# Kernel tuning notes

Hardware: AMD Instinct MI355X
Metric: run time of the kernel (lower is better)

Reference implementation:

```python
import jax, jax.numpy as jnp
import numpy as np
from jax import lax

B, T, H, E, V, ENC = 2048, 48, 512, 256, 128, 1024


def setup_inputs() -> dict:
    key = jax.random.key(0)
    ks = jax.random.split(key, 13)
    s = 0.05  # weight scale to keep activations sane
    return {
        "tgt_ids": jax.random.randint(ks[0], (B, T), 0, V),
        "enc_hid": jax.random.normal(ks[1], (B, ENC), jnp.float32),
        "W_init1": s * jax.random.normal(ks[2], (ENC, H), jnp.float32),
        "W_init2": s * jax.random.normal(ks[3], (ENC, H), jnp.float32),
        "embed_table": s * jax.random.normal(ks[4], (V, E), jnp.float32),
        "k1": s * jax.random.normal(ks[5], (E, 3 * H), jnp.float32),
        "rk1": s * jax.random.normal(ks[6], (H, 3 * H), jnp.float32),
        "b1": jnp.zeros((2, 3 * H), jnp.float32),
        "k2": s * jax.random.normal(ks[7], (H, 3 * H), jnp.float32),
        "rk2": s * jax.random.normal(ks[8], (H, 3 * H), jnp.float32),
        "b2": jnp.zeros((2, 3 * H), jnp.float32),
        "Wv": s * jax.random.normal(ks[9], (H, V), jnp.float32),
        "bv": jnp.zeros((V,), jnp.float32),
    }


def gru_masked(x_proj, mask, h0, rk, rb):
    """Keras GRU (reset_after=True, gate order z,r,h) with mask carry-through.
    x_proj: [B,T,3H] precomputed x@kernel + input_bias. mask: [B,T] bool.
    Masked steps keep previous state AND previous output (Keras masking semantics;
    GRU output == state)."""
    def step(h, inp):
        xg, m = inp  # xg: [B,3H], m: [B]
        inner = h @ rk + rb  # [B,3H]
        xz, xr, xh = jnp.split(xg, 3, axis=-1)
        rz, rr, rh = jnp.split(inner, 3, axis=-1)
        z = jax.nn.sigmoid(xz + rz)
        r = jax.nn.sigmoid(xr + rr)
        hh = jnp.tanh(xh + r * rh)
        h_new = z * h + (1.0 - z) * hh
        h = jnp.where(m[:, None], h_new, h)
        return h, h

    _, seq = lax.scan(step, h0, (x_proj.transpose(1, 0, 2), mask.T))
    return seq.transpose(1, 0, 2)  # [B,T,H]


def reference(tgt_ids, enc_hid, W_init1, W_init2, embed_table,
              k1, rk1, b1, k2, rk2, b2, Wv, bv):
    mask = tgt_ids != 0  # mask_zero=True
    emb = embed_table[tgt_ids]  # [B,T,E]
    h01 = enc_hid @ W_init1  # Dense no-bias init of layer-1 state
    h02 = enc_hid @ W_init2
    x1 = emb @ k1 + b1[0]  # [B,T,3H]
    seq1 = gru_masked(x1, mask, h01, rk1, b1[1])
    x2 = seq1 @ k2 + b2[0]
    seq2 = gru_masked(x2, mask, h02, rk2, b2[1])
    probs = jax.nn.softmax(seq2 @ Wv + bv, axis=-1)  # [B,T,V]
    return probs
```

## Files before the change

kernel.cpp:

```cpp
#include <hip/hip_runtime.h>
#include <hip/hip_bf16.h>
#include <math.h>

#define B_   2048
#define T_   48
#define H_   512
#define E_   256
#define V_   128
#define ENC_ 1024
#define H3_  1536
#define BH_  (B_ * H_)
#define NBLK_ 512

typedef __attribute__((ext_vector_type(8))) short bf16x8;
typedef __attribute__((ext_vector_type(4))) float f32x4;
typedef unsigned short ushort_t;

#if defined(__has_builtin)
#if __has_builtin(__builtin_amdgcn_global_load_lds)
#define HAVE_ASYNC 1
#endif
#endif
#ifndef HAVE_ASYNC
#define HAVE_ASYNC 0
#endif

__device__ __forceinline__ void stage16(const ushort_t* g, ushort_t* l, int lane)
{
#if HAVE_ASYNC
    __builtin_amdgcn_global_load_lds(
        (const __attribute__((address_space(1))) unsigned int*)g,
        (__attribute__((address_space(3))) unsigned int*)l, 16, 0, 0);
#else
    *(bf16x8*)(l + lane * 8) = *(const bf16x8*)g;
#endif
}

__device__ __forceinline__ float sigmoidf_(float x) { return 1.0f / (1.0f + expf(-x)); }

__device__ __forceinline__ void tile_map(int lin, int& m0, int& i0)
{
    const int swz = (lin & 7) * 64 + (lin >> 3);
    m0 = (swz >> 4) * 64;
    i0 = (swz & 15) * 32;
}

constexpr int BM = 64, BN = 64, BK = 16;

__global__ __launch_bounds__(256) void gemm_f32(
    const float* __restrict__ A, const float* __restrict__ Bm,
    const float* __restrict__ bias, float* __restrict__ C,
    int M, int N, int K)
{
    __shared__ float As[BK][BM + 4];
    __shared__ float Bs[BK][BN + 4];

    const int tid = threadIdx.x;
    const int bm = blockIdx.y * BM;
    const int bn = blockIdx.x * BN;
    const int tm = (tid >> 4) * 4;
    const int tn = (tid & 15) * 4;
    const int lmA = tid >> 2;
    const int lkA = (tid & 3) * 4;
    const int lkB = tid >> 4;
    const int lnB = (tid & 15) * 4;

    float acc[4][4] = {};

    for (int k0 = 0; k0 < K; k0 += BK) {
        float4 av  = *(const float4*)(A  + (size_t)(bm + lmA) * K + (k0 + lkA));
        float4 bv4 = *(const float4*)(Bm + (size_t)(k0 + lkB) * N + (bn + lnB));
        As[lkA + 0][lmA] = av.x;
        As[lkA + 1][lmA] = av.y;
        As[lkA + 2][lmA] = av.z;
        As[lkA + 3][lmA] = av.w;
        *(float4*)&Bs[lkB][lnB] = bv4;
        __syncthreads();

        #pragma unroll
        for (int k = 0; k < BK; ++k) {
            float4 a = *(const float4*)&As[k][tm];
            float4 b = *(const float4*)&Bs[k][tn];
            acc[0][0] += a.x * b.x; acc[0][1] += a.x * b.y; acc[0][2] += a.x * b.z; acc[0][3] += a.x * b.w;
            acc[1][0] += a.y * b.x; acc[1][1] += a.y * b.y; acc[1][2] += a.y * b.z; acc[1][3] += a.y * b.w;
            acc[2][0] += a.z * b.x; acc[2][1] += a.z * b.y; acc[2][2] += a.z * b.z; acc[2][3] += a.z * b.w;
            acc[3][0] += a.w * b.x; acc[3][1] += a.w * b.y; acc[3][2] += a.w * b.z; acc[3][3] += a.w * b.w;
        }
        __syncthreads();
    }

    #pragma unroll
    for (int r = 0; r < 4; ++r)
        #pragma unroll
        for (int c = 0; c < 4; ++c) {
            float v = acc[r][c];
            if (bias) v += bias[bn + tn + c];
            C[(size_t)(bm + tm + r) * N + (bn + tn + c)] = v;
        }
}

__global__ __launch_bounds__(256) void transpose_to_bf16(
    const float* __restrict__ W, __hip_bfloat16* __restrict__ Wt, int K, int N)
{
    __shared__ float tile[32][33];
    const int bk = blockIdx.y * 32, bn = blockIdx.x * 32;
    const int tx = threadIdx.x & 31, ty = threadIdx.x >> 5;
    #pragma unroll
    for (int i = ty; i < 32; i += 8)
        tile[i][tx] = W[(size_t)(bk + i) * N + (bn + tx)];
    __syncthreads();
    #pragma unroll
    for (int i = ty; i < 32; i += 8)
        Wt[(size_t)(bn + i) * K + (bk + tx)] = __float2bfloat16(tile[tx][i]);
}

__global__ __launch_bounds__(256) void transpose_split(
    const float* __restrict__ W, __hip_bfloat16* __restrict__ Whi,
    __hip_bfloat16* __restrict__ Wlo, int K, int N)
{
    __shared__ float tile[32][33];
    const int bk = blockIdx.y * 32, bn = blockIdx.x * 32;
    const int tx = threadIdx.x & 31, ty = threadIdx.x >> 5;
    #pragma unroll
    for (int i = ty; i < 32; i += 8)
        tile[i][tx] = W[(size_t)(bk + i) * N + (bn + tx)];
    __syncthreads();
    #pragma unroll
    for (int i = ty; i < 32; i += 8) {
        const float v = tile[tx][i];
        const __hip_bfloat16 h = __float2bfloat16(v);
        Whi[(size_t)(bn + i) * K + (bk + tx)] = h;
        Wlo[(size_t)(bn + i) * K + (bk + tx)] = __float2bfloat16(v - __bfloat162float(h));
    }
}

__global__ __launch_bounds__(256) void split_cast(
    const float* __restrict__ x, __hip_bfloat16* __restrict__ hi,
    __hip_bfloat16* __restrict__ lo, int n)
{
    const int i0 = (blockIdx.x * 256 + threadIdx.x) * 4;
    if (i0 >= n) return;
    const float4 v = *(const float4*)(x + i0);
    const float vv[4] = { v.x, v.y, v.z, v.w };
    #pragma unroll
    for (int j = 0; j < 4; ++j) {
        const __hip_bfloat16 h = __float2bfloat16(vv[j]);
        hi[i0 + j] = h;
        lo[i0 + j] = __float2bfloat16(vv[j] - __bfloat162float(h));
    }
}

__global__ __launch_bounds__(256, 2) void init_mfma(
    const ushort_t* __restrict__ ehi, const ushort_t* __restrict__ elo,
    const ushort_t* __restrict__ w1hi, const ushort_t* __restrict__ w1lo,
    const ushort_t* __restrict__ w2hi, const ushort_t* __restrict__ w2lo,
    float* __restrict__ h1f, __hip_bfloat16* __restrict__ h1b,
    float* __restrict__ h2f, __hip_bfloat16* __restrict__ h2b)
{
    const ushort_t* whi = blockIdx.z ? w2hi : w1hi;
    const ushort_t* wlo = blockIdx.z ? w2lo : w1lo;
    float* hf = blockIdx.z ? h2f : h1f;
    __hip_bfloat16* hb = blockIdx.z ? h2b : h1b;

    __shared__ __attribute__((aligned(16))) ushort_t Ahi[2][4096];
    __shared__ __attribute__((aligned(16))) ushort_t Alo[2][4096];
    __shared__ __attribute__((aligned(16))) ushort_t Bhi[2][2048];
    __shared__ __attribute__((aligned(16))) ushort_t Blo[2][2048];

    const int tid  = threadIdx.x;
    const int lane = tid & 63;
    const int w    = tid >> 6;
    const int ln   = lane & 15;
    const int kg   = lane >> 4;
    const int wr   = w >> 1, wc = w & 1;
    const int m0   = blockIdx.y * 64;
    const int i0   = blockIdx.x * 32;

    const int crow = lane >> 3;
    const int ckof = ((lane & 7) ^ crow) * 8;
    const int ko0 = (kg * 8) ^ ((ln & 7) * 8);
    const int ko1 = (32 + kg * 8) ^ ((ln & 7) * 8);

    auto STG = [&](int pb, int k0) {
        #pragma unroll
        for (int c = w; c < 24; c += 4) {
            const ushort_t* g; ushort_t* l;
            if (c < 8) {
                g = ehi + (size_t)(m0 + c * 8 + crow) * ENC_ + k0 + ckof;
                l = &Ahi[pb][c * 512];
            } else if (c < 16) {
                const int cc = c - 8;
                g = elo + (size_t)(m0 + cc * 8 + crow) * ENC_ + k0 + ckof;
                l = &Alo[pb][cc * 512];
            } else if (c < 20) {
                const int cc = c - 16;
                g = whi + (size_t)(i0 + cc * 8 + crow) * ENC_ + k0 + ckof;
                l = &Bhi[pb][cc * 512];
            } else {
                const int cc = c - 20;
                g = wlo + (size_t)(i0 + cc * 8 + crow) * ENC_ + k0 + ckof;
                l = &Blo[pb][cc * 512];
            }
            stage16(g, l, lane);
        }
    };

    f32x4 acc[2] = {};
    STG(0, 0);
    __syncthreads();
    int buf = 0;
    for (int k0 = 0; k0 < ENC_; k0 += 64) {
        if (k0 + 64 < ENC_) STG(buf ^ 1, k0 + 64);
        #pragma unroll
        for (int kk = 0; kk < 2; ++kk) {
            const int ko = kk ? ko1 : ko0;
            bf16x8 ah[2], al[2], bh, bl;
            #pragma unroll
            for (int fm = 0; fm < 2; ++fm) {
                ah[fm] = *(const bf16x8*)(&Ahi[buf][(wr * 32 + fm * 16 + ln) * 64 + ko]);
                al[fm] = *(const bf16x8*)(&Alo[buf][(wr * 32 + fm * 16 + ln) * 64 + ko]);
            }
            bh = *(const bf16x8*)(&Bhi[buf][(wc * 16 + ln) * 64 + ko]);
            bl = *(const bf16x8*)(&Blo[buf][(wc * 16 + ln) * 64 + ko]);
            #pragma unroll
            for (int fm = 0; fm < 2; ++fm) {
                acc[fm] = __builtin_amdgcn_mfma_f32_16x16x32_bf16(ah[fm], bh, acc[fm], 0, 0, 0);
                acc[fm] = __builtin_amdgcn_mfma_f32_16x16x32_bf16(al[fm], bh, acc[fm], 0, 0, 0);
                acc[fm] = __builtin_amdgcn_mfma_f32_16x16x32_bf16(ah[fm], bl, acc[fm], 0, 0, 0);
            }
        }
        __syncthreads();
        buf ^= 1;
    }

    const int i = i0 + wc * 16 + ln;
    #pragma unroll
    for (int fm = 0; fm < 2; ++fm)
        #pragma unroll
        for (int r = 0; r < 4; ++r) {
            const int b = m0 + wr * 32 + fm * 16 + kg * 4 + r;
            const float v = acc[fm][r];
            hf[(size_t)b * H_ + i] = v;
            hb[(size_t)b * H_ + i] = __float2bfloat16(v);
        }
}

__device__ __forceinline__ void l1_phase(
    ushort_t* Al0, ushort_t* Bl0,
    int m0, int i0, int i, int t,
    const int* __restrict__ tgt, const float* __restrict__ xe1,
    const ushort_t* __restrict__ rkt,
    float rbz, float rbr, float rbh,
    const ushort_t* __restrict__ hb_cur,
    __hip_bfloat16* __restrict__ hb_nxt,
    float (&hv)[2][4])
{
    const int tid  = threadIdx.x;
    const int lane = tid & 63;
    const int w    = tid >> 6;
    const int ln   = lane & 15;
    const int kg   = lane >> 4;
    const int wr   = w >> 1;

    const int crow = lane >> 3;
    const int ckof = ((lane & 7) ^ crow) * 8;

    int ids[2][4];
    #pragma unroll
    for (int fm = 0; fm < 2; ++fm)
        #pragma unroll
        for (int r = 0; r < 4; ++r) {
            const int b = m0 + wr * 32 + fm * 16 + kg * 4 + r;
            ids[fm][r] = tgt[(size_t)b * T_ + t];
        }
    float xgz[2][4], xgr[2][4], xgh[2][4];
    #pragma unroll
    for (int fm = 0; fm < 2; ++fm)
        #pragma unroll
        for (int r = 0; r < 4; ++r) {
            const float* xg = xe1 + (size_t)ids[fm][r] * H3_;
            xgz[fm][r] = xg[i]; xgr[fm][r] = xg[H_ + i]; xgh[fm][r] = xg[2 * H_ + i];
        }

    const int ko0 = (kg * 8) ^ ((ln & 7) * 8);
    const int ko1 = (32 + kg * 8) ^ ((ln & 7) * 8);

    f32x4 acc[2][3] = {};

    auto STAGE = [&](int pb, int k0) {
        #pragma unroll
        for (int c = w; c < 20; c += 4) {
            const ushort_t* g; ushort_t* l;
            if (c < 8) {
                g = hb_cur + (size_t)(m0 + c * 8 + crow) * H_ + k0 + ckof;
                l = Al0 + pb * 4096 + c * 512;
            } else {
                const int idx = c - 8;
                g = rkt + (size_t)((idx >> 2) * H_ + i0 + (idx & 3) * 8 + crow) * H_ + k0 + ckof;
                l = Bl0 + pb * 6144 + idx * 512;
            }
            stage16(g, l, lane);
        }
    };

    STAGE(0, 0);
    __syncthreads();
    int buf = 0;
    for (int k0 = 0; k0 < H_; k0 += 64) {
        if (k0 + 64 < H_) STAGE(buf ^ 1, k0 + 64);
        #pragma unroll
        for (int kk = 0; kk < 2; ++kk) {
            const int ko = kk ? ko1 : ko0;
            bf16x8 af[2], bf[3];
            #pragma unroll
            for (int fm = 0; fm < 2; ++fm)
                af[fm] = *(const bf16x8*)(Al0 + buf * 4096 + (wr * 32 + fm * 16 + ln) * 64 + ko);
            #pragma unroll
            for (int g = 0; g < 3; ++g)
                bf[g] = *(const bf16x8*)(Bl0 + buf * 6144 + g * 2048 + ((w & 1) * 16 + ln) * 64 + ko);
            #pragma unroll
            for (int fm = 0; fm < 2; ++fm)
                #pragma unroll
                for (int g = 0; g < 3; ++g)
                    acc[fm][g] = __builtin_amdgcn_mfma_f32_16x16x32_bf16(
                        af[fm], bf[g], acc[fm][g], 0, 0, 0);
        }
        __syncthreads();
        buf ^= 1;
    }

    #pragma unroll
    for (int fm = 0; fm < 2; ++fm)
        #pragma unroll
        for (int r = 0; r < 4; ++r) {
            const int b = m0 + wr * 32 + fm * 16 + kg * 4 + r;
            const float hvv = hv[fm][r];
            float z  = sigmoidf_(xgz[fm][r] + acc[fm][0][r] + rbz);
            float rr = sigmoidf_(xgr[fm][r] + acc[fm][1][r] + rbr);
            float hh = tanhf(xgh[fm][r] + rr * (acc[fm][2][r] + rbh));
            float hn = (ids[fm][r] != 0) ? (z * hvv + (1.0f - z) * hh) : hvv;
            hv[fm][r] = hn;
            hb_nxt[(size_t)b * H_ + i] = __float2bfloat16(hn);
        }
}

__device__ __forceinline__ void l2_phase(
    ushort_t* lds,
    int m0, int i0, int i, int t,
    const int* __restrict__ tgt,
    const ushort_t* __restrict__ k2t, const ushort_t* __restrict__ rk2t,
    float bxz, float bxr, float bxh,
    float brz, float brr, float brh,
    const ushort_t* __restrict__ s1b,
    const ushort_t* __restrict__ a1, size_t a1s,
    __hip_bfloat16* __restrict__ hbo, size_t hos,
    float (&hv)[2][4])
{
    ushort_t* A0l = lds;
    ushort_t* A1l = lds + 8192;
    ushort_t* B0l = lds + 16384;
    ushort_t* B1l = lds + 22528;

    const int tid  = threadIdx.x;
    const int lane = tid & 63;
    const int w    = tid >> 6;
    const int ln   = lane & 15;
    const int kg   = lane >> 4;
    const int wr   = w >> 1;

    const int crow = lane >> 3;
    const int ckof = ((lane & 7) ^ crow) * 8;

    int ids[2][4];
    #pragma unroll
    for (int fm = 0; fm < 2; ++fm)
        #pragma unroll
        for (int r = 0; r < 4; ++r) {
            const int b = m0 + wr * 32 + fm * 16 + kg * 4 + r;
            ids[fm][r] = tgt[(size_t)b * T_ + t];
        }

    const int ko0 = (kg * 8) ^ ((ln & 7) * 8);
    const int ko1 = (32 + kg * 8) ^ ((ln & 7) * 8);

    auto STAGE_A = [&](int pb, int k0) {
        #pragma unroll
        for (int c = w; c < 16; c += 4) {
            const ushort_t* g; ushort_t* l;
            if (c < 8) {
                g = s1b + (size_t)(m0 + c * 8 + crow) * H_ + k0 + ckof;
                l = A0l + pb * 4096 + c * 512;
            } else {
                const int cc = c - 8;
                g = a1 + (size_t)(m0 + cc * 8 + crow) * a1s + k0 + ckof;
                l = A1l + pb * 4096 + cc * 512;
            }
            stage16(g, l, lane);
        }
    };
    auto STAGE_B = [&](int k0) {
        #pragma unroll
        for (int c = w; c < 24; c += 4) {
            const ushort_t* g; ushort_t* l;
            if (c < 12) {
                g = k2t + (size_t)((c >> 2) * H_ + i0 + (c & 3) * 8 + crow) * H_ + k0 + ckof;
                l = B0l + c * 512;
            } else {
                const int idx = c - 12;
                g = rk2t + (size_t)((idx >> 2) * H_ + i0 + (idx & 3) * 8 + crow) * H_ + k0 + ckof;
                l = B1l + idx * 512;
            }
            stage16(g, l, lane);
        }
    };

    f32x4 acc0[2][3] = {};
    f32x4 acc1[2][3] = {};

    STAGE_A(0, 0);
    STAGE_B(0);
    __syncthreads();
    int buf = 0;
    for (int k0 = 0; k0 < H_; k0 += 64) {
        const bool more = (k0 + 64 < H_);
        if (more) STAGE_A(buf ^ 1, k0 + 64);

        bf16x8 a0f[2][2], a1f[2][2], b0f[2][3], b1f[2][3];
        #pragma unroll
        for (int kk = 0; kk < 2; ++kk) {
            const int ko = kk ? ko1 : ko0;
            #pragma unroll
            for (int fm = 0; fm < 2; ++fm) {
                a0f[kk][fm] = *(const bf16x8*)(A0l + buf * 4096 + (wr * 32 + fm * 16 + ln) * 64 + ko);
                a1f[kk][fm] = *(const bf16x8*)(A1l + buf * 4096 + (wr * 32 + fm * 16 + ln) * 64 + ko);
            }
            #pragma unroll
            for (int g = 0; g < 3; ++g) {
                b0f[kk][g] = *(const bf16x8*)(B0l + g * 2048 + ((w & 1) * 16 + ln) * 64 + ko);
                b1f[kk][g] = *(const bf16x8*)(B1l + g * 2048 + ((w & 1) * 16 + ln) * 64 + ko);
            }
        }
        __builtin_amdgcn_sched_barrier(0);
        asm volatile("s_waitcnt lgkmcnt(0)" ::: "memory");
        __builtin_amdgcn_sched_barrier(0);
        __builtin_amdgcn_s_barrier();
        if (more) STAGE_B(k0 + 64);

        #pragma unroll
        for (int kk = 0; kk < 2; ++kk)
            #pragma unroll
            for (int fm = 0; fm < 2; ++fm)
                #pragma unroll
                for (int g = 0; g < 3; ++g) {
                    acc0[fm][g] = __builtin_amdgcn_mfma_f32_16x16x32_bf16(
                        a0f[kk][fm], b0f[kk][g], acc0[fm][g], 0, 0, 0);
                    acc1[fm][g] = __builtin_amdgcn_mfma_f32_16x16x32_bf16(
                        a1f[kk][fm], b1f[kk][g], acc1[fm][g], 0, 0, 0);
                }
        __syncthreads();
        buf ^= 1;
    }

    #pragma unroll
    for (int fm = 0; fm < 2; ++fm)
        #pragma unroll
        for (int r = 0; r < 4; ++r) {
            const int b = m0 + wr * 32 + fm * 16 + kg * 4 + r;
            const float hvv = hv[fm][r];
            float z  = sigmoidf_((acc0[fm][0][r] + bxz) + (acc1[fm][0][r] + brz));
            float rr = sigmoidf_((acc0[fm][1][r] + bxr) + (acc1[fm][1][r] + brr));
            float hh = tanhf((acc0[fm][2][r] + bxh) + rr * (acc1[fm][2][r] + brh));
            float hn = (ids[fm][r] != 0) ? (z * hvv + (1.0f - z) * hh) : hvv;
            hv[fm][r] = hn;
            hbo[(size_t)b * hos + i] = __float2bfloat16(hn);
        }
}

__global__ __launch_bounds__(256, 2) void l1_fused(
    const int* __restrict__ tgt, int t,
    const float* __restrict__ xe1, const ushort_t* __restrict__ rkt,
    const float* __restrict__ rb,
    const float* __restrict__ hf_cur, const ushort_t* __restrict__ hb_cur,
    float* __restrict__ hf_nxt, __hip_bfloat16* __restrict__ hb_nxt)
{
    __shared__ __attribute__((aligned(16))) ushort_t lds[20480];
    int m0, i0; tile_map(blockIdx.x, m0, i0);
    const int tid = threadIdx.x, lane = tid & 63, w = tid >> 6;
    const int ln = lane & 15, kg = lane >> 4, wr = w >> 1, wc = w & 1;
    const int i = i0 + wc * 16 + ln;

    float hv[2][4];
    #pragma unroll
    for (int fm = 0; fm < 2; ++fm)
        #pragma unroll
        for (int r = 0; r < 4; ++r)
            hv[fm][r] = hf_cur[(size_t)(m0 + wr * 32 + fm * 16 + kg * 4 + r) * H_ + i];

    l1_phase(lds, lds + 8192, m0, i0, i, t, tgt, xe1, rkt,
             rb[i], rb[H_ + i], rb[2 * H_ + i], hb_cur, hb_nxt, hv);

    #pragma unroll
    for (int fm = 0; fm < 2; ++fm)
        #pragma unroll
        for (int r = 0; r < 4; ++r)
            hf_nxt[(size_t)(m0 + wr * 32 + fm * 16 + kg * 4 + r) * H_ + i] = hv[fm][r];
}

__global__ __launch_bounds__(256, 2) void l2_fused(
    const int* __restrict__ tgt, int t,
    const ushort_t* __restrict__ k2t, const ushort_t* __restrict__ rk2t,
    const float* __restrict__ bx, const float* __restrict__ br,
    const ushort_t* __restrict__ s1b,
    const float* __restrict__ hf_cur,
    const ushort_t* __restrict__ hb_cur, size_t hbs,
    float* __restrict__ hf_nxt,
    __hip_bfloat16* __restrict__ hbo, size_t hos)
{
    __shared__ __attribute__((aligned(16))) ushort_t lds[28672];
    int m0, i0; tile_map(blockIdx.x, m0, i0);
    const int tid = threadIdx.x, lane = tid & 63, w = tid >> 6;
    const int ln = lane & 15, kg = lane >> 4, wr = w >> 1, wc = w & 1;
    const int i = i0 + wc * 16 + ln;

    float hv[2][4];
    #pragma unroll
    for (int fm = 0; fm < 2; ++fm)
        #pragma unroll
        for (int r = 0; r < 4; ++r)
            hv[fm][r] = hf_cur[(size_t)(m0 + wr * 32 + fm * 16 + kg * 4 + r) * H_ + i];

    l2_phase(lds, m0, i0, i, t, tgt, k2t, rk2t,
             bx[i], bx[H_ + i], bx[2 * H_ + i],
             br[i], br[H_ + i], br[2 * H_ + i],
             s1b, hb_cur, hbs, hbo, hos, hv);

    #pragma unroll
    for (int fm = 0; fm < 2; ++fm)
        #pragma unroll
        for (int r = 0; r < 4; ++r)
            hf_nxt[(size_t)(m0 + wr * 32 + fm * 16 + kg * 4 + r) * H_ + i] = hv[fm][r];
}

__device__ __forceinline__ void grid_barrier(unsigned* bar, unsigned phase)
{
    __syncthreads();
    if (threadIdx.x == 0) {
        __builtin_amdgcn_fence(__ATOMIC_RELEASE, "agent");
        const unsigned arrived =
            __hip_atomic_fetch_add(&bar[0], 1u, __ATOMIC_RELAXED, __HIP_MEMORY_SCOPE_AGENT) + 1u;
        if (arrived == (unsigned)NBLK_ * (phase + 1u)) {
            __hip_atomic_store(&bar[1], phase + 1u, __ATOMIC_RELAXED, __HIP_MEMORY_SCOPE_AGENT);
        } else {
            while (__hip_atomic_load(&bar[1], __ATOMIC_RELAXED, __HIP_MEMORY_SCOPE_AGENT) < phase + 1u)
                __builtin_amdgcn_s_sleep(4);
        }
        __builtin_amdgcn_fence(__ATOMIC_ACQUIRE, "agent");
    }
    __syncthreads();
}

__global__ __launch_bounds__(256, 2) void recurrence_all(
    const int* __restrict__ tgt, const float* __restrict__ xe1,
    const ushort_t* __restrict__ rk1t, const float* __restrict__ rb1,
    const ushort_t* __restrict__ k2t, const ushort_t* __restrict__ rk2t,
    const float* __restrict__ bx, const float* __restrict__ br,
    const float* __restrict__ h1f0, __hip_bfloat16* __restrict__ h1b,
    const float* __restrict__ h2f0, const __hip_bfloat16* __restrict__ h2b0,
    __hip_bfloat16* __restrict__ seq2b, unsigned* __restrict__ bar)
{
    __shared__ __attribute__((aligned(16))) ushort_t lds[28672];
    int m0, i0; tile_map(blockIdx.x, m0, i0);
    const int tid = threadIdx.x, lane = tid & 63, w = tid >> 6;
    const int ln = lane & 15, kg = lane >> 4, wr = w >> 1, wc = w & 1;
    const int i = i0 + wc * 16 + ln;

    const float rbz = rb1[i], rbr = rb1[H_ + i], rbh = rb1[2 * H_ + i];
    const float bxz = bx[i],  bxr = bx[H_ + i],  bxh = bx[2 * H_ + i];
    const float brz = br[i],  brr = br[H_ + i],  brh = br[2 * H_ + i];

    float hv1[2][4], hv2[2][4];
    #pragma unroll
    for (int fm = 0; fm < 2; ++fm)
        #pragma unroll
        for (int r = 0; r < 4; ++r) {
            const size_t b = (size_t)(m0 + wr * 32 + fm * 16 + kg * 4 + r) * H_ + i;
            hv1[fm][r] = h1f0[b];
            hv2[fm][r] = h2f0[b];
        }

    unsigned ph = 0;

    #pragma unroll 1
    for (int t = 0; t < T_; ++t) {
        const int cur = t & 1, nxt = cur ^ 1;

        l1_phase(lds, lds + 8192, m0, i0, i, t, tgt, xe1, rk1t,
                 rbz, rbr, rbh,
                 (const ushort_t*)(h1b + (size_t)cur * BH_),
                 h1b + (size_t)nxt * BH_, hv1);
        grid_barrier(bar, ph); ++ph;

        const ushort_t* a1 = (t == 0)
            ? (const ushort_t*)h2b0
            : (const ushort_t*)(seq2b + (size_t)(t - 1) * H_);
        const size_t a1s = (t == 0) ? (size_t)H_ : (size_t)T_ * H_;

        l2_phase(lds, m0, i0, i, t, tgt, k2t, rk2t,
                 bxz, bxr, bxh, brz, brr, brh,
                 (const ushort_t*)(h1b + (size_t)nxt * BH_),
                 a1, a1s,
                 seq2b + (size_t)t * H_, (size_t)T_ * H_, hv2);
        if (t + 1 < T_) { grid_barrier(bar, ph); ++ph; }
    }
}

__device__ __forceinline__ void softmax_write4(
    float ax, float ay, float az, float aw, float* __restrict__ outp, int cg)
{
    float m = fmaxf(fmaxf(ax, ay), fmaxf(az, aw));
    #pragma unroll
    for (int d = 16; d >= 1; d >>= 1) m = fmaxf(m, __shfl_xor(m, d));
    float ex = __expf(ax - m), ey = __expf(ay - m),
          ez = __expf(az - m), ew = __expf(aw - m);
    float s = ex + ey + ez + ew;
    #pragma unroll
    for (int d = 16; d >= 1; d >>= 1) s += __shfl_xor(s, d);
    float inv = 1.0f / s;
    float4 o; o.x = ex * inv; o.y = ey * inv; o.z = ez * inv; o.w = ew * inv;
    *(float4*)(outp + cg * 4) = o;
}

__global__ __launch_bounds__(256) void out_softmax(
    const float* __restrict__ h2, const float* __restrict__ Wv,
    const float* __restrict__ bv, float* __restrict__ out, int t)
{
    const int tid = threadIdx.x;
    const int cg = tid & 31;
    const int rg = tid >> 5;
    const int row0 = blockIdx.x * 16;

    __shared__ float hs[16][512];
    for (int idx = tid; idx < 16 * 512; idx += 256)
        hs[idx >> 9][idx & 511] = h2[(size_t)(row0 + (idx >> 9)) * 512 + (idx & 511)];
    __syncthreads();

    const int r0 = rg * 2;
    const float4 bvv = *(const float4*)(bv + cg * 4);
    float a0x = bvv.x, a0y = bvv.y, a0z = bvv.z, a0w = bvv.w;
    float a1x = bvv.x, a1y = bvv.y, a1z = bvv.z, a1w = bvv.w;

    #pragma unroll 4
    for (int k = 0; k < 512; ++k) {
        float4 wv = *(const float4*)(Wv + (size_t)k * V_ + cg * 4);
        float h0 = hs[r0][k], h1 = hs[r0 + 1][k];
        a0x += h0 * wv.x; a0y += h0 * wv.y; a0z += h0 * wv.z; a0w += h0 * wv.w;
        a1x += h1 * wv.x; a1y += h1 * wv.y; a1z += h1 * wv.z; a1w += h1 * wv.w;
    }

    softmax_write4(a0x, a0y, a0z, a0w, out + ((size_t)(row0 + r0) * T_ + t) * V_, cg);
    softmax_write4(a1x, a1y, a1z, a1w, out + ((size_t)(row0 + r0 + 1) * T_ + t) * V_, cg);
}

__global__ __launch_bounds__(256) void proj_mfma(
    const ushort_t* __restrict__ s2, const ushort_t* __restrict__ wvt,
    const float* __restrict__ bv, float* __restrict__ out)
{
    const int lane = threadIdx.x & 63;
    const int w    = threadIdx.x >> 6;
    const int ln   = lane & 15;
    const int kg   = lane >> 4;
    const size_t row0 = (size_t)blockIdx.x * 128 + (size_t)w * 32;

    float bvl[8];
    #pragma unroll
    for (int nf = 0; nf < 8; ++nf) bvl[nf] = bv[nf * 16 + ln];

    f32x4 acc[2][8] = {};
    #pragma unroll 2
    for (int k0 = 0; k0 < H_; k0 += 32) {
        bf16x8 af[2], bf[8];
        #pragma unroll
        for (int mf = 0; mf < 2; ++mf)
            af[mf] = *(const bf16x8*)(s2 + (row0 + mf * 16 + ln) * H_ + k0 + kg * 8);
        #pragma unroll
        for (int nf = 0; nf < 8; ++nf)
            bf[nf] = *(const bf16x8*)(wvt + (size_t)(nf * 16 + ln) * H_ + k0 + kg * 8);
        #pragma unroll
        for (int mf = 0; mf < 2; ++mf)
            #pragma unroll
            for (int nf = 0; nf < 8; ++nf)
                acc[mf][nf] = __builtin_amdgcn_mfma_f32_16x16x32_bf16(
                    af[mf], bf[nf], acc[mf][nf], 0, 0, 0);
    }

    #pragma unroll
    for (int mf = 0; mf < 2; ++mf)
        #pragma unroll
        for (int q = 0; q < 4; ++q) {
            float v[8];
            float m = -1e30f;
            #pragma unroll
            for (int nf = 0; nf < 8; ++nf) { v[nf] = acc[mf][nf][q] + bvl[nf]; m = fmaxf(m, v[nf]); }
            #pragma unroll
            for (int d = 1; d <= 8; d <<= 1) m = fmaxf(m, __shfl_xor(m, d));
            float s = 0.f;
            #pragma unroll
            for (int nf = 0; nf < 8; ++nf) { v[nf] = __expf(v[nf] - m); s += v[nf]; }
            #pragma unroll
            for (int d = 1; d <= 8; d <<= 1) s += __shfl_xor(s, d);
            const float inv = 1.0f / s;
            float* op = out + (row0 + mf * 16 + kg * 4 + q) * V_;
            #pragma unroll
            for (int nf = 0; nf < 8; ++nf) op[nf * 16 + ln] = v[nf] * inv;
        }
}

extern "C" void kernel_launch(void* const* d_in, const int* in_sizes, int n_in,
                              void* d_out, int out_size, void* d_ws, size_t ws_size,
                              hipStream_t stream)
{
    const int*   tgt  = (const int*)  d_in[0];
    const float* enc  = (const float*)d_in[1];
    const float* Wi1  = (const float*)d_in[2];
    const float* Wi2  = (const float*)d_in[3];
    const float* emb  = (const float*)d_in[4];
    const float* k1   = (const float*)d_in[5];
    const float* rk1  = (const float*)d_in[6];
    const float* b1   = (const float*)d_in[7];
    const float* k2   = (const float*)d_in[8];
    const float* rk2  = (const float*)d_in[9];
    const float* b2   = (const float*)d_in[10];
    const float* Wv   = (const float*)d_in[11];
    const float* bv   = (const float*)d_in[12];
    float* out = (float*)d_out;

    float* ws  = (float*)d_ws;
    float* xe1 = ws;
    float* h1f = xe1 + (size_t)V_ * H3_;
    float* h2f = h1f + (size_t)2 * BH_;
    __hip_bfloat16* h1b = (__hip_bfloat16*)(h2f + (size_t)2 * BH_);
    __hip_bfloat16* h2b = h1b + (size_t)2 * BH_;
    __hip_bfloat16* rk1t = h2b + (size_t)2 * BH_;
    __hip_bfloat16* k2t  = rk1t + (size_t)H3_ * H_;
    __hip_bfloat16* rk2t = k2t  + (size_t)H3_ * H_;
    __hip_bfloat16* wvt  = rk2t + (size_t)H3_ * H_;
    __hip_bfloat16* ehi  = wvt + (size_t)V_ * H_;
    __hip_bfloat16* elo  = ehi + (size_t)B_ * ENC_;
    __hip_bfloat16* w1hi = elo + (size_t)B_ * ENC_;
    __hip_bfloat16* w1lo = w1hi + (size_t)H_ * ENC_;
    __hip_bfloat16* w2hi = w1lo + (size_t)H_ * ENC_;
    __hip_bfloat16* w2lo = w2hi + (size_t)H_ * ENC_;
    __hip_bfloat16* seq2b = w2lo + (size_t)H_ * ENC_;
    unsigned* bar = (unsigned*)(seq2b + (size_t)B_ * T_ * H_);

    const size_t need = (size_t)((char*)bar + 64 - (char*)d_ws);
    const bool batched = ws_size >= need;

    static int persist_state = -1;
    if (persist_state < 0) {
        int nb = 0;
        hipError_t e1 = hipOccupancyMaxActiveBlocksPerMultiprocessor(&nb, recurrence_all, 256, 0);
        hipDeviceProp_t prop;
        hipError_t e2 = hipGetDeviceProperties(&prop, 0);
        persist_state = (e1 == hipSuccess && e2 == hipSuccess &&
                         (long)nb * prop.multiProcessorCount >= NBLK_) ? 1 : 0;
    }
    const bool persist = batched && persist_state == 1;

    dim3 blk(256);

    transpose_to_bf16<<<dim3(H3_ / 32, H_ / 32), blk, 0, stream>>>(rk1, rk1t, H_, H3_);
    transpose_to_bf16<<<dim3(H3_ / 32, H_ / 32), blk, 0, stream>>>(k2,  k2t,  H_, H3_);
    transpose_to_bf16<<<dim3(H3_ / 32, H_ / 32), blk, 0, stream>>>(rk2, rk2t, H_, H3_);
    if (batched)
        transpose_to_bf16<<<dim3(V_ / 32, H_ / 32), blk, 0, stream>>>(Wv, wvt, H_, V_);

    split_cast<<<dim3((B_ * ENC_) / 1024), blk, 0, stream>>>(enc, ehi, elo, B_ * ENC_);
    transpose_split<<<dim3(H_ / 32, ENC_ / 32), blk, 0, stream>>>(Wi1, w1hi, w1lo, ENC_, H_);
    transpose_split<<<dim3(H_ / 32, ENC_ / 32), blk, 0, stream>>>(Wi2, w2hi, w2lo, ENC_, H_);

    gemm_f32<<<dim3(H3_ / BN, V_ / BM), blk, 0, stream>>>(emb, k1, b1, xe1, V_, H3_, E_);

    init_mfma<<<dim3(H_ / 32, B_ / 64, 2), blk, 0, stream>>>(
        (const ushort_t*)ehi, (const ushort_t*)elo,
        (const ushort_t*)w1hi, (const ushort_t*)w1lo,
        (const ushort_t*)w2hi, (const ushort_t*)w2lo,
        h1f, h1b, h2f, h2b);

    if (persist) {
        hipMemsetAsync(bar, 0, 64, stream);
        recurrence_all<<<dim3(NBLK_), blk, 0, stream>>>(
            tgt, xe1, (const ushort_t*)rk1t, b1 + H3_,
            (const ushort_t*)k2t, (const ushort_t*)rk2t, b2, b2 + H3_,
            h1f, h1b, h2f, h2b, seq2b, bar);
        proj_mfma<<<dim3((B_ * T_) / 128), blk, 0, stream>>>(
            (const ushort_t*)seq2b, (const ushort_t*)wvt, bv, out);
        return;
    }

    const dim3 fgrid(NBLK_);
    for (int t = 0; t < T_; ++t) {
        const int cur = t & 1, nxt = cur ^ 1;
        float* h1f_c = h1f + (size_t)cur * BH_;
        float* h1f_n = h1f + (size_t)nxt * BH_;
        float* h2f_c = h2f + (size_t)cur * BH_;
        float* h2f_n = h2f + (size_t)nxt * BH_;
        __hip_bfloat16* h1b_c = h1b + (size_t)cur * BH_;
        __hip_bfloat16* h1b_n = h1b + (size_t)nxt * BH_;

        l1_fused<<<fgrid, blk, 0, stream>>>(
            tgt, t, xe1, (const ushort_t*)rk1t, b1 + H3_,
            h1f_c, (const ushort_t*)h1b_c, h1f_n, h1b_n);

        const ushort_t* hb_c; size_t hbs;
        __hip_bfloat16* hbo; size_t hos;
        if (batched) {
            hb_c = (t == 0) ? (const ushort_t*)h2b
                            : (const ushort_t*)(seq2b + (size_t)(t - 1) * H_);
            hbs  = (t == 0) ? (size_t)H_ : (size_t)T_ * H_;
            hbo  = seq2b + (size_t)t * H_;
            hos  = (size_t)T_ * H_;
        } else {
            hb_c = (const ushort_t*)(h2b + (size_t)cur * BH_); hbs = H_;
            hbo  = h2b + (size_t)nxt * BH_;                    hos = H_;
        }

        l2_fused<<<fgrid, blk, 0, stream>>>(
            tgt, t, (const ushort_t*)k2t, (const ushort_t*)rk2t, b2, b2 + H3_,
            (const ushort_t*)h1b_n, h2f_c, hb_c, hbs, h2f_n, hbo, hos);

        if (!batched)
            out_softmax<<<dim3(B_ / 16), blk, 0, stream>>>(h2f_n, Wv, bv, out, t);
    }

    if (batched)
        proj_mfma<<<dim3((B_ * T_) / 128), blk, 0, stream>>>(
            (const ushort_t*)seq2b, (const ushort_t*)wvt, bv, out);
}
```

Before: 1.515 ms.

## Replace grid-barrier fences with cache-bypassing loads/stores and remap tile ordering

The recurrent state (hidden bf16 buffers) is now read with global_load sc0 sc1 through registers and written with sc0 sc1 stores, which bypass non-coherent caches. This allows the agent-scope release/acquire fences in the persistent grid barrier to be removed and replaced by a vmcnt(0) wait. The A-operand staging also moves from async global-to-LDS loads to register loads with explicit vmcnt waits, and the block-to-tile mapping changes so neighbouring blocks share row tiles. The risk is memory-ordering correctness, because it now depends on the cache-control bits and on the waitcnt counts, which must exactly match the number of outstanding loads.

```diff
diff --git a/kernel.cpp b/kernel.cpp
--- a/kernel.cpp
+++ b/kernel.cpp
@@ -36,13 +36,32 @@
 #endif
 }
 
+__device__ __forceinline__ bf16x8 load16_sc(const ushort_t* g)
+{
+    bf16x8 r;
+    asm volatile("global_load_dwordx4 %0, %1, off sc0 sc1" : "=v"(r) : "v"(g));
+    return r;
+}
+
+__device__ __forceinline__ void store_bf16_sc(__hip_bfloat16* p, float v)
+{
+    union { __hip_bfloat16 h; unsigned short u; } cv;
+    cv.h = __float2bfloat16(v);
+    unsigned uv = cv.u;
+    asm volatile("global_store_short %0, %1, off sc0 sc1" :: "v"(p), "v"(uv) : "memory");
+}
+
+__device__ __forceinline__ void wait_vm3()
+{ asm volatile("s_waitcnt vmcnt(3)" ::: "memory"); __builtin_amdgcn_sched_barrier(0); }
+__device__ __forceinline__ void wait_vm6()
+{ asm volatile("s_waitcnt vmcnt(6)" ::: "memory"); __builtin_amdgcn_sched_barrier(0); }
+
 __device__ __forceinline__ float sigmoidf_(float x) { return 1.0f / (1.0f + expf(-x)); }
 
 __device__ __forceinline__ void tile_map(int lin, int& m0, int& i0)
 {
-    const int swz = (lin & 7) * 64 + (lin >> 3);
-    m0 = (swz >> 4) * 64;
-    i0 = (swz & 15) * 32;
+    i0 = ((((lin & 7) << 1) | ((lin >> 3) & 1))) * 32;
+    m0 = (lin >> 4) * 64;
 }
 
 constexpr int BM = 64, BN = 64, BK = 16;
@@ -286,28 +305,38 @@
     const int ko1 = (32 + kg * 8) ^ ((ln & 7) * 8);
 
     f32x4 acc[2][3] = {};
-
-    auto STAGE = [&](int pb, int k0) {
-        #pragma unroll
-        for (int c = w; c < 20; c += 4) {
-            const ushort_t* g; ushort_t* l;
-            if (c < 8) {
-                g = hb_cur + (size_t)(m0 + c * 8 + crow) * H_ + k0 + ckof;
-                l = Al0 + pb * 4096 + c * 512;
-            } else {
-                const int idx = c - 8;
-                g = rkt + (size_t)((idx >> 2) * H_ + i0 + (idx & 3) * 8 + crow) * H_ + k0 + ckof;
-                l = Bl0 + pb * 6144 + idx * 512;
-            }
-            stage16(g, l, lane);
+    bf16x8 areg[2];
+
+    auto LOAD_A = [&](int k0) {
+        #pragma unroll
+        for (int c2 = 0; c2 < 2; ++c2) {
+            const int c = w + c2 * 4;
+            areg[c2] = load16_sc(hb_cur + (size_t)(m0 + c * 8 + crow) * H_ + k0 + ckof);
         }
     };
-
-    STAGE(0, 0);
+    auto STORE_A = [&](int pb) {
+        #pragma unroll
+        for (int c2 = 0; c2 < 2; ++c2) {
+            const int c = w + c2 * 4;
+            *(bf16x8*)(Al0 + pb * 4096 + c * 512 + lane * 8) = areg[c2];
+        }
+    };
+    auto STAGE_B = [&](int pb, int k0) {
+        #pragma unroll
+        for (int idx = w; idx < 12; idx += 4)
+            stage16(rkt + (size_t)((idx >> 2) * H_ + i0 + (idx & 3) * 8 + crow) * H_ + k0 + ckof,
+                    Bl0 + pb * 6144 + idx * 512, lane);
+    };
+
+    LOAD_A(0);
+    STAGE_B(0, 0);
+    wait_vm3();
+    STORE_A(0);
     __syncthreads();
     int buf = 0;
     for (int k0 = 0; k0 < H_; k0 += 64) {
-        if (k0 + 64 < H_) STAGE(buf ^ 1, k0 + 64);
+        const bool more = (k0 + 64 < H_);
+        if (more) { LOAD_A(k0 + 64); STAGE_B(buf ^ 1, k0 + 64); }
         #pragma unroll
         for (int kk = 0; kk < 2; ++kk) {
             const int ko = kk ? ko1 : ko0;
@@ -325,6 +354,7 @@
                     acc[fm][g] = __builtin_amdgcn_mfma_f32_16x16x32_bf16(
                         af[fm], bf[g], acc[fm][g], 0, 0, 0);
         }
+        if (more) { wait_vm3(); STORE_A(buf ^ 1); }
         __syncthreads();
         buf ^= 1;
     }
@@ -340,7 +370,7 @@
             float hh = tanhf(xgh[fm][r] + rr * (acc[fm][2][r] + rbh));
             float hn = (ids[fm][r] != 0) ? (z * hvv + (1.0f - z) * hh) : hvv;
             hv[fm][r] = hn;
-            hb_nxt[(size_t)b * H_ + i] = __float2bfloat16(hn);
+            store_bf16_sc(hb_nxt + (size_t)b * H_ + i, hn);
         }
 }
 
@@ -383,19 +413,25 @@
     const int ko0 = (kg * 8) ^ ((ln & 7) * 8);
     const int ko1 = (32 + kg * 8) ^ ((ln & 7) * 8);
 
-    auto STAGE_A = [&](int pb, int k0) {
-        #pragma unroll
-        for (int c = w; c < 16; c += 4) {
-            const ushort_t* g; ushort_t* l;
-            if (c < 8) {
-                g = s1b + (size_t)(m0 + c * 8 + crow) * H_ + k0 + ckof;
-                l = A0l + pb * 4096 + c * 512;
-            } else {
-                const int cc = c - 8;
-                g = a1 + (size_t)(m0 + cc * 8 + crow) * a1s + k0 + ckof;
-                l = A1l + pb * 4096 + cc * 512;
-            }
-            stage16(g, l, lane);
+    bf16x8 areg[4];
+
+    auto LOAD_A = [&](int k0) {
+        #pragma unroll
+        for (int c2 = 0; c2 < 4; ++c2) {
+            const int c = w + c2 * 4;
+            const ushort_t* g = (c < 8)
+                ? s1b + (size_t)(m0 + c * 8 + crow) * H_ + k0 + ckof
+                : a1  + (size_t)(m0 + (c - 8) * 8 + crow) * a1s + k0 + ckof;
+            areg[c2] = load16_sc(g);
+        }
+    };
+    auto STORE_A = [&](int pb) {
+        #pragma unroll
+        for (int c2 = 0; c2 < 4; ++c2) {
+            const int c = w + c2 * 4;
+            ushort_t* l = (c < 8) ? A0l + pb * 4096 + c * 512
+                                  : A1l + pb * 4096 + (c - 8) * 512;
+            *(bf16x8*)(l + lane * 8) = areg[c2];
         }
     };
     auto STAGE_B = [&](int k0) {
@@ -417,13 +453,15 @@
     f32x4 acc0[2][3] = {};
     f32x4 acc1[2][3] = {};
 
-    STAGE_A(0, 0);
+    LOAD_A(0);
     STAGE_B(0);
+    wait_vm6();
+    STORE_A(0);
     __syncthreads();
     int buf = 0;
     for (int k0 = 0; k0 < H_; k0 += 64) {
         const bool more = (k0 + 64 < H_);
-        if (more) STAGE_A(buf ^ 1, k0 + 64);
+        if (more) LOAD_A(k0 + 64);
 
         bf16x8 a0f[2][2], a1f[2][2], b0f[2][3], b1f[2][3];
         #pragma unroll
@@ -457,6 +495,7 @@
                     acc1[fm][g] = __builtin_amdgcn_mfma_f32_16x16x32_bf16(
                         a1f[kk][fm], b1f[kk][g], acc1[fm][g], 0, 0, 0);
                 }
+        if (more) { wait_vm6(); STORE_A(buf ^ 1); }
         __syncthreads();
         buf ^= 1;
     }
@@ -472,7 +511,7 @@
             float hh = tanhf((acc0[fm][2][r] + bxh) + rr * (acc1[fm][2][r] + brh));
             float hn = (ids[fm][r] != 0) ? (z * hvv + (1.0f - z) * hh) : hvv;
             hv[fm][r] = hn;
-            hbo[(size_t)b * hos + i] = __float2bfloat16(hn);
+            store_bf16_sc(hbo + (size_t)b * hos + i, hn);
         }
 }
 
@@ -543,9 +582,9 @@
 
 __device__ __forceinline__ void grid_barrier(unsigned* bar, unsigned phase)
 {
+    asm volatile("s_waitcnt vmcnt(0)" ::: "memory");
     __syncthreads();
     if (threadIdx.x == 0) {
-        __builtin_amdgcn_fence(__ATOMIC_RELEASE, "agent");
         const unsigned arrived =
             __hip_atomic_fetch_add(&bar[0], 1u, __ATOMIC_RELAXED, __HIP_MEMORY_SCOPE_AGENT) + 1u;
         if (arrived == (unsigned)NBLK_ * (phase + 1u)) {
@@ -554,7 +593,6 @@
             while (__hip_atomic_load(&bar[1], __ATOMIC_RELAXED, __HIP_MEMORY_SCOPE_AGENT) < phase + 1u)
                 __builtin_amdgcn_s_sleep(4);
         }
-        __builtin_amdgcn_fence(__ATOMIC_ACQUIRE, "agent");
     }
     __syncthreads();
 }
```

New measurement: 1.435 ms. 5.2% less time.
